# Optimization experiments

Measured on AMD Instinct MI355X. Metric: run time of the kernel, lower is better.

The kernel has to match this reference:

```python
import jax, jax.numpy as jnp
import numpy as np
from jax import lax

IMG_H, IMG_W = 800, 800           # self.image_size
GRID = 64                         # feature map H=W
STRIDE = IMG_H // GRID            # torchvision AnchorGenerator stride
ANCHOR_SIZE = 32.0                # sizes=(32,), aspect_ratios=(1.0,)
PRE_NMS_TOP_N = 500
POST_NMS_TOP_N = 500
NMS_THRESH = 0.7
MIN_BOX_SIZE = 0.001
MIN_BOX_SCORE = 0.0


def make_anchors(h, w, stride):
    # torchvision single-size, ratio-1 base anchor centered at origin: [-16,-16,16,16]
    half = ANCHOR_SIZE / 2.0
    base = jnp.array([-half, -half, half, half], dtype=jnp.float32)
    sx = jnp.arange(w, dtype=jnp.float32) * stride
    sy = jnp.arange(h, dtype=jnp.float32) * stride
    yy, xx = jnp.meshgrid(sy, sx, indexing='ij')
    shifts = jnp.stack([xx, yy, xx, yy], axis=-1).reshape(-1, 4)  # [HW,4], row-major over (y,x)
    return shifts + base  # [HW,4] in (x1,y1,x2,y2)


def decode_boxes(reg, anchors):
    # reg: [B,N,4] (dx,dy,dw,dh); anchors: [N,4]
    wa = anchors[:, 2] - anchors[:, 0]
    ha = anchors[:, 3] - anchors[:, 1]
    cxa = anchors[:, 0] + 0.5 * wa
    cya = anchors[:, 1] + 0.5 * ha
    dx, dy, dw, dh = reg[..., 0], reg[..., 1], reg[..., 2], reg[..., 3]
    cx = dx * wa + cxa
    cy = dy * ha + cya
    w = jnp.exp(dw) * wa
    h = jnp.exp(dh) * ha
    return jnp.stack([cx - 0.5 * w, cy - 0.5 * h, cx + 0.5 * w, cy + 0.5 * h], axis=-1)


def clip_boxes(boxes):
    x = jnp.clip(boxes[..., 0::2], 0.0, float(IMG_W))
    y = jnp.clip(boxes[..., 1::2], 0.0, float(IMG_H))
    out = jnp.stack([x[..., 0], y[..., 0], x[..., 1], y[..., 1]], axis=-1)
    return out


def pairwise_iou(boxes):
    # boxes: [N,4] -> iou [N,N]
    area = (boxes[:, 2] - boxes[:, 0]) * (boxes[:, 3] - boxes[:, 1])
    lt = jnp.maximum(boxes[:, None, :2], boxes[None, :, :2])
    rb = jnp.minimum(boxes[:, None, 2:], boxes[None, :, 2:])
    wh = jnp.clip(rb - lt, 0.0)
    inter = wh[..., 0] * wh[..., 1]
    return inter / (area[:, None] + area[None, :] - inter + 1e-9)


def nms_keep(boxes, valid):
    # boxes already sorted by descending score (topk output). Greedy NMS.
    n = boxes.shape[0]
    iou = pairwise_iou(boxes)
    idx = jnp.arange(n)

    def body(i, keep):
        suppress = keep[i] & (iou[i] > NMS_THRESH) & (idx > i)
        return keep & jnp.logical_not(suppress)

    return lax.fori_loop(0, n, body, valid)


def setup_inputs() -> dict:
    key = jax.random.key(0)
    ks = jax.random.split(key, 4)
    B, C, H, W = 4, 512, GRID, GRID
    feature_map = jax.random.normal(ks[0], (B, C, H, W), dtype=jnp.float32)
    conv_w = jax.random.normal(ks[1], (512, 512, 3, 3), dtype=jnp.float32) * 0.02
    conv_b = jnp.zeros((512,), dtype=jnp.float32)
    score_w = jax.random.normal(ks[2], (1, 512), dtype=jnp.float32) * 0.01
    score_b = jnp.zeros((1,), dtype=jnp.float32)
    bbox_w = jax.random.normal(ks[3], (4, 512), dtype=jnp.float32) * 0.01
    bbox_b = jnp.zeros((4,), dtype=jnp.float32)
    return {"feature_map": feature_map, "conv_w": conv_w, "conv_b": conv_b,
            "score_w": score_w, "score_b": score_b, "bbox_w": bbox_w, "bbox_b": bbox_b}


def reference(feature_map, conv_w, conv_b, score_w, score_b, bbox_w, bbox_b):
    B, C, H, W = feature_map.shape
    # common_feature_extractor: 3x3 conv + ReLU
    f = lax.conv_general_dilated(feature_map, conv_w, (1, 1), 'SAME',
                                 dimension_numbers=('NCHW', 'OIHW', 'NCHW'))
    f = jax.nn.relu(f + conv_b[None, :, None, None])
    # 1x1 heads
    object_score = jnp.einsum('bchw,oc->bohw', f, score_w) + score_b[None, :, None, None]  # [B,1,H,W]
    bbox_reg = jnp.einsum('bchw,oc->bohw', f, bbox_w) + bbox_b[None, :, None, None]        # [B,4,H,W]
    # reshape (B,4,-1).permute(0,2,1) -> [B,N,4]
    reg = jnp.transpose(bbox_reg.reshape(B, 4, -1), (0, 2, 1))
    anchors = make_anchors(H, W, STRIDE)                 # [N,4]
    proposals = decode_boxes(reg, anchors)               # [B,N,4]
    logits = object_score.reshape(B, -1)                 # [B,N]
    # filter_proposals: topk on detached logits
    top_vals, top_idx = lax.top_k(lax.stop_gradient(logits), PRE_NMS_TOP_N)  # sorted desc
    props = jnp.take_along_axis(proposals, top_idx[..., None], axis=1)       # [B,500,4]
    probs = jax.nn.sigmoid(top_vals)                                          # [B,500]
    props = clip_boxes(props)
    ws = props[..., 2] - props[..., 0]
    hs = props[..., 3] - props[..., 1]
    valid = (ws >= MIN_BOX_SIZE) & (hs >= MIN_BOX_SIZE) & (probs >= MIN_BOX_SCORE)
    keep = jax.vmap(nms_keep)(props, valid)               # [B,500] (post_nms_top_n == pre, no truncation)
    final_props = props * keep[..., None].astype(props.dtype)
    final_scores = probs * keep.astype(probs.dtype)
    return f, final_props, final_scores, keep
```

## Files before the change

### kernel.cpp

```cpp
#include <hip/hip_runtime.h>
#include <math.h>

#define BB   4
#define CC   512
#define HH   64
#define WW   64
#define NN   4096
#define TOPK 500

typedef _Float16 half8 __attribute__((ext_vector_type(8)));
typedef float f32x16   __attribute__((ext_vector_type(16)));

__device__ __forceinline__ void split_f16(float v, _Float16& h, _Float16& l) {
    h = (_Float16)v;
    l = (_Float16)(v - (float)h);
}

__global__ __launch_bounds__(256) void prepack_w_kernel(
    const float* __restrict__ w, _Float16* __restrict__ wh,
    _Float16* __restrict__ wl)
{
    const int t = blockIdx.x * 256 + threadIdx.x;
    if (t >= 512 * 32) return;
    const int co = t & 511;
    const int cb = t >> 9;
    const float* src = w + (size_t)co * 4608 + cb * 144;
#pragma unroll
    for (int tap = 0; tap < 9; ++tap) {
        half8 h0, h1, l0, l1;
#pragma unroll
        for (int i = 0; i < 8; ++i) {
            _Float16 h, l;
            split_f16(src[i * 9 + tap] * 4096.0f, h, l);
            h0[i] = h; l0[i] = l;
            split_f16(src[(i + 8) * 9 + tap] * 4096.0f, h, l);
            h1[i] = h; l1[i] = l;
        }
        const size_t dst = ((size_t)(tap * 32 + cb) * 512 + co) * 16;
        *(half8*)(wh + dst)     = h0;
        *(half8*)(wh + dst + 8) = h1;
        *(half8*)(wl + dst)     = l0;
        *(half8*)(wl + dst + 8) = l1;
    }
}

__global__ __launch_bounds__(256, 2) void conv3x3_mfma_kernel(
    const float* __restrict__ x, const _Float16* __restrict__ wh,
    const _Float16* __restrict__ wl, const float* __restrict__ bias,
    float* __restrict__ out)
{
    __shared__ __align__(16) _Float16 xs_h[2][4][66][24];
    __shared__ __align__(16) _Float16 xs_l[2][4][66][24];

    const int tid  = threadIdx.x;
    const int lane = tid & 63;
    const int wave = tid >> 6;
    const int wco  = wave & 1;
    const int wpx  = wave >> 1;
    const int kg   = lane >> 5;
    const int ln   = lane & 31;

    const int co_blk = blockIdx.x * 128;
    const int r0     = blockIdx.y * 2;
    const int b      = blockIdx.z;

    const float* xb = x + (size_t)b * CC * NN;

    const int s_ci   = tid & 15;
    const int s_sub  = tid >> 4;
    const int s_row  = s_sub & 3;
    const int s_colg = s_sub >> 2;
    const int gr     = r0 - 1 + s_row;
    const bool gr_ok = ((unsigned)gr < 64u);
    const float* xrow = xb + (size_t)s_ci * NN + gr * 64 + s_colg * 16;

    if (tid < 128) {
        const int ci = tid & 15, rr = (tid >> 4) & 3, side = (tid >> 6) & 1;
        xs_h[0][rr][side * 65][ci] = (_Float16)0.f;
        xs_l[0][rr][side * 65][ci] = (_Float16)0.f;
        xs_h[1][rr][side * 65][ci] = (_Float16)0.f;
        xs_l[1][rr][side * 65][ci] = (_Float16)0.f;
    }

    f32x16 acc[2][2];
#pragma unroll
    for (int mt = 0; mt < 2; ++mt)
#pragma unroll
        for (int nt = 0; nt < 2; ++nt)
#pragma unroll
            for (int r = 0; r < 16; ++r) acc[mt][nt][r] = 0.f;

    half8 Ah[2][2], Al[2][2];
    half8 Bh[2][2], Bl[2][2];

    const int co_w0  = co_blk + wco * 64 + ln;
    const size_t aoff0 = (size_t)co_w0 * 16 + kg * 8;
    const size_t aoff1 = aoff0 + 32 * 16;

    float vals[16];
#pragma unroll
    for (int j = 0; j < 16; ++j) vals[j] = 0.f;

    if (gr_ok) {
        *(float4*)&vals[0]  = *(const float4*)(xrow + 0);
        *(float4*)&vals[4]  = *(const float4*)(xrow + 4);
        *(float4*)&vals[8]  = *(const float4*)(xrow + 8);
        *(float4*)&vals[12] = *(const float4*)(xrow + 12);
    }
#pragma unroll
    for (int j = 0; j < 16; ++j) {
        _Float16 h, l;
        split_f16(vals[j] * 4096.0f, h, l);
        const int c = 1 + s_colg * 16 + j;
        xs_h[0][s_row][c][s_ci] = h;
        xs_l[0][s_row][c][s_ci] = l;
    }
    __syncthreads();
    int buf = 0;

    for (int cb = 0; cb < 32; ++cb) {
        {
            const size_t ab = (size_t)(0 * 32 + cb) * 8192;
            Ah[0][0] = *(const half8*)(wh + ab + aoff0);
            Al[0][0] = *(const half8*)(wl + ab + aoff0);
            Ah[0][1] = *(const half8*)(wh + ab + aoff1);
            Al[0][1] = *(const half8*)(wl + ab + aoff1);
            Bh[0][0] = *(const half8*)&xs_h[buf][wpx][ln][kg * 8];
            Bl[0][0] = *(const half8*)&xs_l[buf][wpx][ln][kg * 8];
            Bh[0][1] = *(const half8*)&xs_h[buf][wpx][32 + ln][kg * 8];
            Bl[0][1] = *(const half8*)&xs_l[buf][wpx][32 + ln][kg * 8];
        }
#pragma unroll
        for (int tap = 0; tap < 9; ++tap) {
            const int pb = tap & 1, pn = pb ^ 1;
            if (tap < 8) {
                const int t1 = tap + 1;
                const size_t ab = (size_t)(t1 * 32 + cb) * 8192;
                Ah[pn][0] = *(const half8*)(wh + ab + aoff0);
                Al[pn][0] = *(const half8*)(wl + ab + aoff0);
                Ah[pn][1] = *(const half8*)(wh + ab + aoff1);
                Al[pn][1] = *(const half8*)(wl + ab + aoff1);
                const int dy1 = t1 / 3, dx1 = t1 % 3;
                Bh[pn][0] = *(const half8*)&xs_h[buf][wpx + dy1][ln + dx1][kg * 8];
                Bl[pn][0] = *(const half8*)&xs_l[buf][wpx + dy1][ln + dx1][kg * 8];
                Bh[pn][1] = *(const half8*)&xs_h[buf][wpx + dy1][32 + ln + dx1][kg * 8];
                Bl[pn][1] = *(const half8*)&xs_l[buf][wpx + dy1][32 + ln + dx1][kg * 8];
            }
            if (tap == 7 && cb < 31 && gr_ok) {
                const float* p = xrow + (size_t)(cb + 1) * 16 * NN;
                *(float4*)&vals[0]  = *(const float4*)(p + 0);
                *(float4*)&vals[4]  = *(const float4*)(p + 4);
                *(float4*)&vals[8]  = *(const float4*)(p + 8);
                *(float4*)&vals[12] = *(const float4*)(p + 12);
            }
#pragma unroll
            for (int mt = 0; mt < 2; ++mt)
#pragma unroll
                for (int nt = 0; nt < 2; ++nt) {
                    acc[mt][nt] = __builtin_amdgcn_mfma_f32_32x32x16_f16(
                        Al[pb][mt], Bh[pb][nt], acc[mt][nt], 0, 0, 0);
                    acc[mt][nt] = __builtin_amdgcn_mfma_f32_32x32x16_f16(
                        Ah[pb][mt], Bl[pb][nt], acc[mt][nt], 0, 0, 0);
                    acc[mt][nt] = __builtin_amdgcn_mfma_f32_32x32x16_f16(
                        Ah[pb][mt], Bh[pb][nt], acc[mt][nt], 0, 0, 0);
                }
        }
        if (cb < 31) {
            const int nb = buf ^ 1;
#pragma unroll
            for (int j = 0; j < 16; ++j) {
                _Float16 h, l;
                split_f16(vals[j] * 4096.0f, h, l);
                const int c = 1 + s_colg * 16 + j;
                xs_h[nb][s_row][c][s_ci] = h;
                xs_l[nb][s_row][c][s_ci] = l;
            }
            __syncthreads();
            buf = nb;
        }
    }

    const float inv_scale = 5.9604644775390625e-08f;
    const int himg = r0 + wpx;
#pragma unroll
    for (int mt = 0; mt < 2; ++mt)
#pragma unroll
        for (int nt = 0; nt < 2; ++nt) {
            const int wimg = nt * 32 + ln;
#pragma unroll
            for (int reg = 0; reg < 16; ++reg) {
                const int co = co_blk + wco * 64 + mt * 32 +
                               (reg & 3) + 8 * (reg >> 2) + 4 * kg;
                float v = fmaf(acc[mt][nt][reg], inv_scale, bias[co]);
                v = v > 0.f ? v : 0.f;
                out[(((size_t)b * CC + co) * HH + himg) * WW + wimg] = v;
            }
        }
}

__global__ __launch_bounds__(256) void conv3x3_relu_kernel(
    const float* __restrict__ x, const float* __restrict__ wgt,
    const float* __restrict__ bias, float* __restrict__ out)
{
    __shared__ float xs[8][6][66];
    __shared__ float wsh[8][9][64];
    const int co_base = blockIdx.x * 64;
    const int r0 = blockIdx.y * 4;
    const int b  = blockIdx.z;
    const int tid = threadIdx.x;
    const int col = tid & 63;
    const int co_off = (tid >> 6) * 16;

    float acc[4][16];
#pragma unroll
    for (int r = 0; r < 4; ++r)
#pragma unroll
        for (int k = 0; k < 16; ++k) acc[r][k] = 0.f;

    const float* xb = x + (size_t)b * CC * HH * WW;

    for (int cb = 0; cb < CC; cb += 8) {
        __syncthreads();
        for (int idx = tid; idx < 8 * 6 * 66; idx += 256) {
            int cc = idx % 66;
            int rest = idx / 66;
            int rr = rest % 6;
            int ci = rest / 6;
            int gr = r0 - 1 + rr;
            int gc = cc - 1;
            float v = 0.f;
            if (gr >= 0 && gr < HH && (unsigned)gc < (unsigned)WW)
                v = xb[((cb + ci) * HH + gr) * WW + gc];
            xs[ci][rr][cc] = v;
        }
        for (int idx = tid; idx < 8 * 9 * 64; idx += 256) {
            int co = idx & 63;
            int rest = idx >> 6;
            int ci = rest / 9;
            int tap = rest - ci * 9;
            wsh[ci][tap][co] = wgt[(size_t)(co_base + co) * (CC * 9) + (cb + ci) * 9 + tap];
        }
        __syncthreads();
#pragma unroll
        for (int ci = 0; ci < 8; ++ci) {
#pragma unroll
            for (int kh = 0; kh < 3; ++kh) {
                float xv[4][3];
#pragma unroll
                for (int r = 0; r < 4; ++r)
#pragma unroll
                    for (int kw = 0; kw < 3; ++kw)
                        xv[r][kw] = xs[ci][r + kh][col + kw];
#pragma unroll
                for (int kw = 0; kw < 3; ++kw) {
#pragma unroll
                    for (int k = 0; k < 16; k += 4) {
                        float4 wv = *(const float4*)&wsh[ci][kh * 3 + kw][co_off + k];
#pragma unroll
                        for (int r = 0; r < 4; ++r) {
                            acc[r][k + 0] = fmaf(xv[r][kw], wv.x, acc[r][k + 0]);
                            acc[r][k + 1] = fmaf(xv[r][kw], wv.y, acc[r][k + 1]);
                            acc[r][k + 2] = fmaf(xv[r][kw], wv.z, acc[r][k + 2]);
                            acc[r][k + 3] = fmaf(xv[r][kw], wv.w, acc[r][k + 3]);
                        }
                    }
                }
            }
        }
    }
#pragma unroll
    for (int k = 0; k < 16; ++k) {
        const int co = co_base + co_off + k;
        const float bv = bias[co];
#pragma unroll
        for (int r = 0; r < 4; ++r) {
            float v = acc[r][k] + bv;
            v = v > 0.f ? v : 0.f;
            out[(((size_t)b * CC + co) * HH + (r0 + r)) * WW + col] = v;
        }
    }
}

__global__ __launch_bounds__(64) void heads_decode_kernel(
    const float* __restrict__ f, const float* __restrict__ score_w,
    const float* __restrict__ score_b, const float* __restrict__ bbox_w,
    const float* __restrict__ bbox_b,
    float* __restrict__ logits, float* __restrict__ props)
{
    __shared__ float sw[CC];
    __shared__ float bw0[CC], bw1[CC], bw2[CC], bw3[CC];
    const int tid = threadIdx.x;
    for (int i = tid; i < CC; i += 64) {
        sw[i]  = score_w[i];
        bw0[i] = bbox_w[0 * CC + i];
        bw1[i] = bbox_w[1 * CC + i];
        bw2[i] = bbox_w[2 * CC + i];
        bw3[i] = bbox_w[3 * CC + i];
    }
    __syncthreads();
    const int b = blockIdx.y;
    const int n = blockIdx.x * 64 + tid;
    const float* fb = f + (size_t)b * CC * NN + n;
    float s = 0.f, d0 = 0.f, d1 = 0.f, d2 = 0.f, d3 = 0.f;
    for (int ci = 0; ci < CC; ++ci) {
        float v = fb[(size_t)ci * NN];
        s  = fmaf(v, sw[ci],  s);
        d0 = fmaf(v, bw0[ci], d0);
        d1 = fmaf(v, bw1[ci], d1);
        d2 = fmaf(v, bw2[ci], d2);
        d3 = fmaf(v, bw3[ci], d3);
    }
    s  += score_b[0];
    d0 += bbox_b[0]; d1 += bbox_b[1]; d2 += bbox_b[2]; d3 += bbox_b[3];
    logits[b * NN + n] = s;
    const int hx = n & 63, hy = n >> 6;
    const float cxa = 12.f * (float)hx, cya = 12.f * (float)hy;
    const float cx = d0 * 32.f + cxa;
    const float cy = d1 * 32.f + cya;
    const float w2 = expf(d2) * 16.f;
    const float h2 = expf(d3) * 16.f;
    float* p = props + ((size_t)b * NN + n) * 4;
    p[0] = cx - w2; p[1] = cy - h2; p[2] = cx + w2; p[3] = cy + h2;
}

__global__ __launch_bounds__(1024) void topk_kernel(
    const float* __restrict__ logits, const float* __restrict__ props,
    float* __restrict__ props500, float* __restrict__ probs500,
    unsigned long long* __restrict__ validb)
{
    __shared__ unsigned long long skey[NN];
    const int b = blockIdx.x;
    const int tid = threadIdx.x;
    for (int i = tid; i < NN; i += 1024) {
        const unsigned u = __float_as_uint(logits[b * NN + i]);
        const unsigned k32 = u ^ ((u >> 31) ? 0xFFFFFFFFu : 0x80000000u);
        skey[i] = ((unsigned long long)k32 << 32) | (unsigned)(NN - 1 - i);
    }
    __syncthreads();
    for (int k = 2; k <= NN; k <<= 1) {
        for (int j = k >> 1; j > 0; j >>= 1) {
            for (int t = tid; t < NN / 2; t += 1024) {
                const int i = ((t & ~(j - 1)) << 1) | (t & (j - 1));
                const int l = i | j;
                const unsigned long long a = skey[i], c = skey[l];
                const bool bef  = (a > c);
                const bool swap = ((i & k) == 0) ? !bef : bef;
                if (swap) { skey[i] = c; skey[l] = a; }
            }
            __syncthreads();
        }
    }
    if (tid < 512) {
        bool val = false;
        if (tid < TOPK) {
            const unsigned long long K = skey[tid];
            const int n = NN - 1 - (int)(K & 0xFFFFFFFFu);
            const unsigned k32 = (unsigned)(K >> 32);
            const unsigned u = (k32 & 0x80000000u) ? (k32 ^ 0x80000000u) : ~k32;
            const float v = __uint_as_float(u);
            const float* p = props + ((size_t)b * NN + n) * 4;
            const float x1 = fminf(fmaxf(p[0], 0.f), 800.f);
            const float y1 = fminf(fmaxf(p[1], 0.f), 800.f);
            const float x2 = fminf(fmaxf(p[2], 0.f), 800.f);
            const float y2 = fminf(fmaxf(p[3], 0.f), 800.f);
            const float pr = 1.f / (1.f + expf(-v));
            float* q = props500 + ((size_t)b * TOPK + tid) * 4;
            q[0] = x1; q[1] = y1; q[2] = x2; q[3] = y2;
            probs500[b * TOPK + tid] = pr;
            val = ((x2 - x1) >= 0.001f) && ((y2 - y1) >= 0.001f) && (pr >= 0.f);
        }
        const unsigned long long m = __ballot(val);
        if ((tid & 63) == 0) validb[b * 8 + (tid >> 6)] = m;
    }
}

__global__ __launch_bounds__(256) void nms_mask_kernel(
    const float* __restrict__ props500, unsigned long long* __restrict__ mask)
{
    const int gid = blockIdx.x * 256 + threadIdx.x;
    if (gid >= BB * TOPK * 8) return;
    const int wword = gid & 7;
    const int rest = gid >> 3;
    const int i = rest % TOPK;
    const int b = rest / TOPK;
    const float* bp = props500 + (size_t)b * TOPK * 4;
    const float x1 = bp[i * 4 + 0], y1 = bp[i * 4 + 1];
    const float x2 = bp[i * 4 + 2], y2 = bp[i * 4 + 3];
    const float ai = (x2 - x1) * (y2 - y1);
    unsigned long long m = 0ull;
    for (int bit = 0; bit < 64; ++bit) {
        const int j = wword * 64 + bit;
        if (j >= TOPK) break;
        if (j <= i) continue;
        const float u1 = bp[j * 4 + 0], v1 = bp[j * 4 + 1];
        const float u2 = bp[j * 4 + 2], v2 = bp[j * 4 + 3];
        const float aj = (u2 - u1) * (v2 - v1);
        const float lx = fmaxf(x1, u1), ly = fmaxf(y1, v1);
        const float rx = fminf(x2, u2), ry = fminf(y2, v2);
        const float iw = fmaxf(rx - lx, 0.f), ih = fmaxf(ry - ly, 0.f);
        const float inter = iw * ih;
        const float iou = inter / (ai + aj - inter + 1e-9f);
        if (iou > 0.7f) m |= (1ull << bit);
    }
    mask[gid] = m;
}

__global__ __launch_bounds__(256) void nms_finalize_kernel(
    const unsigned long long* __restrict__ mask,
    const unsigned long long* __restrict__ validb,
    const float* __restrict__ props500, const float* __restrict__ probs500,
    float* __restrict__ out_props, float* __restrict__ out_scores,
    float* __restrict__ out_keep)
{
    __shared__ unsigned long long sm[TOPK * 8];
    __shared__ unsigned long long sk[8];
    const int b = blockIdx.x;
    const int tid = threadIdx.x;
    for (int i = tid; i < TOPK * 8; i += 256) sm[i] = mask[(size_t)b * TOPK * 8 + i];
    if (tid < 8) sk[tid] = validb[b * 8 + tid];
    __syncthreads();
    if (tid == 0) {
        unsigned long long kw[8];
#pragma unroll
        for (int w = 0; w < 8; ++w) kw[w] = sk[w];
#pragma unroll
        for (int wi = 0; wi < 8; ++wi) {
            const int lim = (wi == 7) ? (TOPK - 7 * 64) : 64;
            for (int bi = 0; bi < lim; ++bi) {
                const unsigned long long keepbit = (kw[wi] >> bi) & 1ull;
                const unsigned long long sel = 0ull - keepbit;
                const int i = wi * 64 + bi;
#pragma unroll
                for (int w = 0; w < 8; ++w) kw[w] &= ~(sm[i * 8 + w] & sel);
            }
        }
#pragma unroll
        for (int w = 0; w < 8; ++w) sk[w] = kw[w];
    }
    __syncthreads();
    for (int t = tid; t < TOPK; t += 256) {
        const float fk = (float)((sk[t >> 6] >> (t & 63)) & 1ull);
        const float* q = props500 + ((size_t)b * TOPK + t) * 4;
        float* o = out_props + ((size_t)b * TOPK + t) * 4;
        o[0] = q[0] * fk; o[1] = q[1] * fk; o[2] = q[2] * fk; o[3] = q[3] * fk;
        out_scores[b * TOPK + t] = probs500[b * TOPK + t] * fk;
        out_keep[b * TOPK + t]   = fk;
    }
}

extern "C" void kernel_launch(void* const* d_in, const int* in_sizes, int n_in,
                              void* d_out, int out_size, void* d_ws, size_t ws_size,
                              hipStream_t stream)
{
    const float* x       = (const float*)d_in[0];
    const float* conv_w  = (const float*)d_in[1];
    const float* conv_b  = (const float*)d_in[2];
    const float* score_w = (const float*)d_in[3];
    const float* score_b = (const float*)d_in[4];
    const float* bbox_w  = (const float*)d_in[5];
    const float* bbox_b  = (const float*)d_in[6];

    float* f_out      = (float*)d_out;
    float* out_props  = f_out + (size_t)BB * CC * HH * WW;
    float* out_scores = out_props + BB * TOPK * 4;
    float* out_keep   = out_scores + BB * TOPK;

    const size_t WPE = (size_t)9 * 32 * 512 * 16;
    const size_t WP_BYTES = WPE * 2 * sizeof(_Float16);
    const size_t SCRATCH_BYTES =
        (size_t)BB * NN * 4 + (size_t)BB * NN * 16 + (size_t)BB * TOPK * 16 +
        (size_t)BB * TOPK * 4 + (size_t)BB * 8 * 8 + (size_t)BB * TOPK * 8 * 8 + 256;
    const bool use_mfma = (ws_size >= WP_BYTES + SCRATCH_BYTES);

    _Float16* wph = (_Float16*)d_ws;
    _Float16* wpl = wph + WPE;
    char* scratch = use_mfma ? (char*)(wpl + WPE) : (char*)d_ws;

    float* logits   = (float*)scratch;
    float* props    = logits + BB * NN;
    float* props500 = props + BB * NN * 4;
    float* probs500 = props500 + BB * TOPK * 4;
    unsigned long long* validb = (unsigned long long*)(probs500 + BB * TOPK);
    unsigned long long* maskp  = validb + BB * 8;

    if (use_mfma) {
        prepack_w_kernel<<<64, 256, 0, stream>>>(conv_w, wph, wpl);
        conv3x3_mfma_kernel<<<dim3(4, 32, BB), 256, 0, stream>>>(x, wph, wpl, conv_b, f_out);
    } else {
        conv3x3_relu_kernel<<<dim3(8, 16, BB), 256, 0, stream>>>(x, conv_w, conv_b, f_out);
    }
    heads_decode_kernel<<<dim3(64, BB), 64, 0, stream>>>(f_out, score_w, score_b,
                                                         bbox_w, bbox_b, logits, props);
    topk_kernel<<<BB, 1024, 0, stream>>>(logits, props, props500, probs500, validb);
    nms_mask_kernel<<<(BB * TOPK * 8 + 255) / 256, 256, 0, stream>>>(props500, maskp);
    nms_finalize_kernel<<<BB, 256, 0, stream>>>(maskp, validb, props500, probs500,
                                                out_props, out_scores, out_keep);
}
```

Before: 458.0 us.

## Fuse top-k, NMS mask and finalize into one per-batch kernel

```diff
diff --git a/kernel.cpp b/kernel.cpp
--- a/kernel.cpp
+++ b/kernel.cpp
@@ -120,7 +120,7 @@
 
     for (int cb = 0; cb < 32; ++cb) {
         {
-            const size_t ab = (size_t)(0 * 32 + cb) * 8192;
+            const size_t ab = (size_t)cb * 8192;
             Ah[0][0] = *(const half8*)(wh + ab + aoff0);
             Al[0][0] = *(const half8*)(wl + ab + aoff0);
             Ah[0][1] = *(const half8*)(wh + ab + aoff1);
@@ -302,6 +302,7 @@
     const int n = blockIdx.x * 64 + tid;
     const float* fb = f + (size_t)b * CC * NN + n;
     float s = 0.f, d0 = 0.f, d1 = 0.f, d2 = 0.f, d3 = 0.f;
+#pragma unroll 8
     for (int ci = 0; ci < CC; ++ci) {
         float v = fb[(size_t)ci * NN];
         s  = fmaf(v, sw[ci],  s);
@@ -323,18 +324,22 @@
     p[0] = cx - w2; p[1] = cy - h2; p[2] = cx + w2; p[3] = cy + h2;
 }
 
-__global__ __launch_bounds__(1024) void topk_kernel(
+__global__ __launch_bounds__(1024) void topk_nms_kernel(
     const float* __restrict__ logits, const float* __restrict__ props,
-    float* __restrict__ props500, float* __restrict__ probs500,
-    unsigned long long* __restrict__ validb)
-{
-    __shared__ unsigned long long skey[NN];
+    float* __restrict__ out_props, float* __restrict__ out_scores,
+    float* __restrict__ out_keep)
+{
+    __shared__ unsigned long long smem[NN];
+    __shared__ float pbox[TOPK][4];
+    __shared__ float pprob[TOPK];
+    __shared__ unsigned long long sk[8];
     const int b = blockIdx.x;
     const int tid = threadIdx.x;
+
     for (int i = tid; i < NN; i += 1024) {
         const unsigned u = __float_as_uint(logits[b * NN + i]);
         const unsigned k32 = u ^ ((u >> 31) ? 0xFFFFFFFFu : 0x80000000u);
-        skey[i] = ((unsigned long long)k32 << 32) | (unsigned)(NN - 1 - i);
+        smem[i] = ((unsigned long long)k32 << 32) | (unsigned)(NN - 1 - i);
     }
     __syncthreads();
     for (int k = 2; k <= NN; k <<= 1) {
@@ -342,10 +347,10 @@
             for (int t = tid; t < NN / 2; t += 1024) {
                 const int i = ((t & ~(j - 1)) << 1) | (t & (j - 1));
                 const int l = i | j;
-                const unsigned long long a = skey[i], c = skey[l];
+                const unsigned long long a = smem[i], c = smem[l];
                 const bool bef  = (a > c);
                 const bool swap = ((i & k) == 0) ? !bef : bef;
-                if (swap) { skey[i] = c; skey[l] = a; }
+                if (swap) { smem[i] = c; smem[l] = a; }
             }
             __syncthreads();
         }
@@ -353,7 +358,7 @@
     if (tid < 512) {
         bool val = false;
         if (tid < TOPK) {
-            const unsigned long long K = skey[tid];
+            const unsigned long long K = smem[tid];
             const int n = NN - 1 - (int)(K & 0xFFFFFFFFu);
             const unsigned k32 = (unsigned)(K >> 32);
             const unsigned u = (k32 & 0x80000000u) ? (k32 ^ 0x80000000u) : ~k32;
@@ -364,86 +369,55 @@
             const float x2 = fminf(fmaxf(p[2], 0.f), 800.f);
             const float y2 = fminf(fmaxf(p[3], 0.f), 800.f);
             const float pr = 1.f / (1.f + expf(-v));
-            float* q = props500 + ((size_t)b * TOPK + tid) * 4;
-            q[0] = x1; q[1] = y1; q[2] = x2; q[3] = y2;
-            probs500[b * TOPK + tid] = pr;
+            pbox[tid][0] = x1; pbox[tid][1] = y1;
+            pbox[tid][2] = x2; pbox[tid][3] = y2;
+            pprob[tid] = pr;
             val = ((x2 - x1) >= 0.001f) && ((y2 - y1) >= 0.001f) && (pr >= 0.f);
         }
         const unsigned long long m = __ballot(val);
-        if ((tid & 63) == 0) validb[b * 8 + (tid >> 6)] = m;
-    }
-}
-
-__global__ __launch_bounds__(256) void nms_mask_kernel(
-    const float* __restrict__ props500, unsigned long long* __restrict__ mask)
-{
-    const int gid = blockIdx.x * 256 + threadIdx.x;
-    if (gid >= BB * TOPK * 8) return;
-    const int wword = gid & 7;
-    const int rest = gid >> 3;
-    const int i = rest % TOPK;
-    const int b = rest / TOPK;
-    const float* bp = props500 + (size_t)b * TOPK * 4;
-    const float x1 = bp[i * 4 + 0], y1 = bp[i * 4 + 1];
-    const float x2 = bp[i * 4 + 2], y2 = bp[i * 4 + 3];
-    const float ai = (x2 - x1) * (y2 - y1);
-    unsigned long long m = 0ull;
-    for (int bit = 0; bit < 64; ++bit) {
-        const int j = wword * 64 + bit;
-        if (j >= TOPK) break;
-        if (j <= i) continue;
-        const float u1 = bp[j * 4 + 0], v1 = bp[j * 4 + 1];
-        const float u2 = bp[j * 4 + 2], v2 = bp[j * 4 + 3];
-        const float aj = (u2 - u1) * (v2 - v1);
-        const float lx = fmaxf(x1, u1), ly = fmaxf(y1, v1);
-        const float rx = fminf(x2, u2), ry = fminf(y2, v2);
-        const float iw = fmaxf(rx - lx, 0.f), ih = fmaxf(ry - ly, 0.f);
-        const float inter = iw * ih;
-        const float iou = inter / (ai + aj - inter + 1e-9f);
-        if (iou > 0.7f) m |= (1ull << bit);
-    }
-    mask[gid] = m;
-}
-
-__global__ __launch_bounds__(256) void nms_finalize_kernel(
-    const unsigned long long* __restrict__ mask,
-    const unsigned long long* __restrict__ validb,
-    const float* __restrict__ props500, const float* __restrict__ probs500,
-    float* __restrict__ out_props, float* __restrict__ out_scores,
-    float* __restrict__ out_keep)
-{
-    __shared__ unsigned long long sm[TOPK * 8];
-    __shared__ unsigned long long sk[8];
-    const int b = blockIdx.x;
-    const int tid = threadIdx.x;
-    for (int i = tid; i < TOPK * 8; i += 256) sm[i] = mask[(size_t)b * TOPK * 8 + i];
-    if (tid < 8) sk[tid] = validb[b * 8 + tid];
-    __syncthreads();
-    if (tid == 0) {
-        unsigned long long kw[8];
-#pragma unroll
-        for (int w = 0; w < 8; ++w) kw[w] = sk[w];
-#pragma unroll
-        for (int wi = 0; wi < 8; ++wi) {
-            const int lim = (wi == 7) ? (TOPK - 7 * 64) : 64;
-            for (int bi = 0; bi < lim; ++bi) {
-                const unsigned long long keepbit = (kw[wi] >> bi) & 1ull;
-                const unsigned long long sel = 0ull - keepbit;
-                const int i = wi * 64 + bi;
-#pragma unroll
-                for (int w = 0; w < 8; ++w) kw[w] &= ~(sm[i * 8 + w] & sel);
-            }
-        }
-#pragma unroll
-        for (int w = 0; w < 8; ++w) sk[w] = kw[w];
-    }
-    __syncthreads();
-    for (int t = tid; t < TOPK; t += 256) {
+        if ((tid & 63) == 0) sk[tid >> 6] = m;
+    }
+    __syncthreads();
+    for (int idx = tid; idx < TOPK * 8; idx += 1024) {
+        const int i = idx >> 3, w = idx & 7;
+        const float x1 = pbox[i][0], y1 = pbox[i][1];
+        const float x2 = pbox[i][2], y2 = pbox[i][3];
+        const float ai = (x2 - x1) * (y2 - y1);
+        unsigned long long m = 0ull;
+#pragma unroll 4
+        for (int bit = 0; bit < 64; ++bit) {
+            const int j = w * 64 + bit;
+            if (j >= TOPK) break;
+            if (j <= i) continue;
+            const float u1 = pbox[j][0], v1 = pbox[j][1];
+            const float u2 = pbox[j][2], v2 = pbox[j][3];
+            const float aj = (u2 - u1) * (v2 - v1);
+            const float lx = fmaxf(x1, u1), ly = fmaxf(y1, v1);
+            const float rx = fminf(x2, u2), ry = fminf(y2, v2);
+            const float iw = fmaxf(rx - lx, 0.f), ih = fmaxf(ry - ly, 0.f);
+            const float inter = iw * ih;
+            const float iou = inter / (ai + aj - inter + 1e-9f);
+            if (iou > 0.7f) m |= (1ull << bit);
+        }
+        smem[idx] = m;
+    }
+    __syncthreads();
+    if (tid < 8) {
+        unsigned long long kw = sk[tid];
+        for (int i = 0; i < TOPK; ++i) {
+            const unsigned long long kwi = __shfl(kw, i >> 6);
+            if ((kwi >> (i & 63)) & 1ull)
+                kw &= ~smem[i * 8 + tid];
+        }
+        sk[tid] = kw;
+    }
+    __syncthreads();
+    for (int t = tid; t < TOPK; t += 1024) {
         const float fk = (float)((sk[t >> 6] >> (t & 63)) & 1ull);
-        const float* q = props500 + ((size_t)b * TOPK + t) * 4;
         float* o = out_props + ((size_t)b * TOPK + t) * 4;
-        o[0] = q[0] * fk; o[1] = q[1] * fk; o[2] = q[2] * fk; o[3] = q[3] * fk;
-        out_scores[b * TOPK + t] = probs500[b * TOPK + t] * fk;
+        o[0] = pbox[t][0] * fk; o[1] = pbox[t][1] * fk;
+        o[2] = pbox[t][2] * fk; o[3] = pbox[t][3] * fk;
+        out_scores[b * TOPK + t] = pprob[t] * fk;
         out_keep[b * TOPK + t]   = fk;
     }
 }
@@ -467,21 +441,15 @@
 
     const size_t WPE = (size_t)9 * 32 * 512 * 16;
     const size_t WP_BYTES = WPE * 2 * sizeof(_Float16);
-    const size_t SCRATCH_BYTES =
-        (size_t)BB * NN * 4 + (size_t)BB * NN * 16 + (size_t)BB * TOPK * 16 +
-        (size_t)BB * TOPK * 4 + (size_t)BB * 8 * 8 + (size_t)BB * TOPK * 8 * 8 + 256;
+    const size_t SCRATCH_BYTES = (size_t)BB * NN * 4 + (size_t)BB * NN * 16 + 256;
     const bool use_mfma = (ws_size >= WP_BYTES + SCRATCH_BYTES);
 
     _Float16* wph = (_Float16*)d_ws;
     _Float16* wpl = wph + WPE;
     char* scratch = use_mfma ? (char*)(wpl + WPE) : (char*)d_ws;
 
-    float* logits   = (float*)scratch;
-    float* props    = logits + BB * NN;
-    float* props500 = props + BB * NN * 4;
-    float* probs500 = props500 + BB * TOPK * 4;
-    unsigned long long* validb = (unsigned long long*)(probs500 + BB * TOPK);
-    unsigned long long* maskp  = validb + BB * 8;
+    float* logits = (float*)scratch;
+    float* props  = logits + BB * NN;
 
     if (use_mfma) {
         prepack_w_kernel<<<64, 256, 0, stream>>>(conv_w, wph, wpl);
@@ -491,8 +459,6 @@
     }
     heads_decode_kernel<<<dim3(64, BB), 64, 0, stream>>>(f_out, score_w, score_b,
                                                          bbox_w, bbox_b, logits, props);
-    topk_kernel<<<BB, 1024, 0, stream>>>(logits, props, props500, probs500, validb);
-    nms_mask_kernel<<<(BB * TOPK * 8 + 255) / 256, 256, 0, stream>>>(props500, maskp);
-    nms_finalize_kernel<<<BB, 256, 0, stream>>>(maskp, validb, props500, probs500,
-                                                out_props, out_scores, out_keep);
-}
+    topk_nms_kernel<<<BB, 1024, 0, stream>>>(logits, props,
+                                             out_props, out_scores, out_keep);
+}
```

Result: slower. 474.1 us (+3.5%).
